# Kernel tuning notes

Hardware: AMD Instinct MI355X
Metric: run time of the kernel (lower is better)

Reference implementation:

```python
import jax, jax.numpy as jnp
import numpy as np

V, E, H, B, S = 50000, 256, 256, 64, 2048


def setup_inputs() -> dict:
    key = jax.random.key(0)
    ks = jax.random.split(key, 13)
    u = lambda k, shape: jax.random.uniform(k, shape, jnp.float32) - 0.5
    return {
        "inp": jax.random.randint(ks[0], (B,), 0, V, dtype=jnp.int64),
        "hidden": jax.random.normal(ks[1], (1, B, H), jnp.float32),
        "encoder_outputs": jax.random.normal(ks[2], (B, S, H), jnp.float32),
        "emb": jax.random.normal(ks[3], (V, E), jnp.float32),          # nn.Embedding weight
        "U": u(ks[4], (H, H)),
        "W": u(ks[5], (H, H)),
        "v": u(ks[6], (H, 1)),
        "W_ih": u(ks[7], (H, E)),   # RNN weight_ih_l0
        "W_hh": u(ks[8], (H, H)),   # RNN weight_hh_l0
        "b_ih": u(ks[9], (H,)),
        "b_hh": u(ks[10], (H,)),
        "W_out": u(ks[11], (V, H)),  # output Linear weight
        "b_out": u(ks[12], (V,)),
    }


def reference(inp, hidden, encoder_outputs, emb, U, W, v,
              W_ih, W_hh, b_ih, b_hh, W_out, b_out):
    # embedding lookup: (B, E)
    x = emb[inp]
    word_embs = x[:, None, :]                         # (B, 1, E)
    # Bahdanau additive attention (get_context)
    summed = jnp.tanh(word_embs @ U + encoder_outputs @ W)   # (B, S, H)
    e_ij = summed @ v                                        # (B, S, 1)
    alpha = jax.nn.softmax(e_ij, axis=1)                     # (B, S, 1)
    context = jnp.sum(alpha * encoder_outputs, axis=1)       # (B, H)
    # single tanh-RNN step; NOTE: original code feeds context as initial hidden,
    # ignoring the `hidden` argument when attention is enabled.
    h_new = jnp.tanh(x @ W_ih.T + b_ih + context @ W_hh.T + b_hh)  # (B, H)
    logits = h_new @ W_out.T + b_out                               # (B, V)
    return logits, h_new[None]                                     # hidden: (1, B, H)
```

## Files before the change

### kernel.cpp

```cpp
#include <hip/hip_runtime.h>
#include <hip/hip_bf16.h>
#include <math.h>

#define V_ 50000
#define E_ 256
#define H_ 256
#define B_ 64
#define S_ 2048
#define NCHK 32

typedef __attribute__((ext_vector_type(4))) float f32x4;
typedef __attribute__((ext_vector_type(16))) float f32x16;
typedef __attribute__((ext_vector_type(8))) __bf16 bf16x8;

static __device__ __forceinline__ f32x4 mfma16(bf16x8 a, bf16x8 b, f32x4 c) {
  return __builtin_amdgcn_mfma_f32_16x16x32_bf16(a, b, c, 0, 0, 0);
}
static __device__ __forceinline__ f32x16 mfma32(bf16x8 a, bf16x8 b, f32x16 c) {
  return __builtin_amdgcn_mfma_f32_32x32x16_bf16(a, b, c, 0, 0, 0);
}
static __device__ __forceinline__ float fast_tanh(float x) {
  const float e2 = __expf(2.0f * x);
  return 1.0f - 2.0f / (e2 + 1.0f);
}

__global__ __launch_bounds__(256) void prep_k(
    const int* __restrict__ inp, const float* __restrict__ emb,
    const float* __restrict__ U, const float* __restrict__ W_ih,
    const float* __restrict__ b_ih, const float* __restrict__ b_hh,
    float* __restrict__ xU, float* __restrict__ xWih) {
  const int b = blockIdx.x, h = threadIdx.x;
  __shared__ float xs[H_];
  xs[h] = emb[(size_t)inp[b] * E_ + h];
  __syncthreads();
  float au = 0.f, aw = 0.f;
  const float* __restrict__ wir = W_ih + (size_t)h * E_;
  for (int k = 0; k < H_; k += 4) {
    const float4 x4 = *reinterpret_cast<const float4*>(&xs[k]);
    const float4 w4 = *reinterpret_cast<const float4*>(wir + k);
    aw = fmaf(x4.x, w4.x, aw); aw = fmaf(x4.y, w4.y, aw);
    aw = fmaf(x4.z, w4.z, aw); aw = fmaf(x4.w, w4.w, aw);
    au = fmaf(x4.x, U[(size_t)(k + 0) * H_ + h], au);
    au = fmaf(x4.y, U[(size_t)(k + 1) * H_ + h], au);
    au = fmaf(x4.z, U[(size_t)(k + 2) * H_ + h], au);
    au = fmaf(x4.w, U[(size_t)(k + 3) * H_ + h], au);
  }
  xU[b * H_ + h] = au;
  xWih[b * H_ + h] = aw + b_ih[h] + b_hh[h];
}

__global__ __launch_bounds__(256) void prep_w(
    const float* __restrict__ W, __bf16* __restrict__ wt2) {
  const int idx = blockIdx.x * 256 + threadIdx.x;
  const int k = idx >> 8, col = idx & 255;
  wt2[((size_t)(k >> 3) * 256 + col) * 8 + (k & 7)] = (__bf16)W[(size_t)k * H_ + col];
}

__global__ __launch_bounds__(512, 4) void attn_fused(
    const float* __restrict__ enc, const __bf16* __restrict__ wt2,
    const float* __restrict__ xU, const float* __restrict__ vv,
    float* __restrict__ ctxp, float* __restrict__ mlout) {
  const int t = threadIdx.x;
  const int w = t >> 6, l = t & 63, l31 = l & 31, h5 = l >> 5;
  const int rg = w >> 1, cg = w & 1;

  __shared__ float ered[2][128];
  __shared__ float wgt[2][64];
  __shared__ float mlL[2][2];

  const int ridx = blockIdx.x;
  const int b = blockIdx.y;
  const int s0 = ridx * 128;

  const float* __restrict__ encA =
      enc + ((size_t)b * S_ + s0 + rg * 32 + l31) * H_ + h5 * 8;

  f32x16 acc[4];
#pragma unroll
  for (int cf = 0; cf < 4; ++cf) acc[cf] = (f32x16)(0.f);

  float4 af[2][2];
  af[0][0] = *reinterpret_cast<const float4*>(encA);
  af[0][1] = *reinterpret_cast<const float4*>(encA + 4);
  af[1][0] = *reinterpret_cast<const float4*>(encA + 16);
  af[1][1] = *reinterpret_cast<const float4*>(encA + 20);

#pragma unroll
  for (int ks = 0; ks < 16; ++ks) {
    const int ca = ks & 1;
    bf16x8 ahi, alo;
    {
      const float4 c0 = af[ca][0], c1 = af[ca][1];
      const float xa[8] = {c0.x, c0.y, c0.z, c0.w, c1.x, c1.y, c1.z, c1.w};
#pragma unroll
      for (int j = 0; j < 8; ++j) {
        const __bf16 hh = (__bf16)xa[j];
        ahi[j] = hh;
        alo[j] = (__bf16)(xa[j] - (float)hh);
      }
    }
    if (ks < 14) {
      af[ca][0] = *reinterpret_cast<const float4*>(encA + (ks + 2) * 16);
      af[ca][1] = *reinterpret_cast<const float4*>(encA + (ks + 2) * 16 + 4);
    }
    bf16x8 bb[4];
    const int koct = ks * 2 + h5;
#pragma unroll
    for (int cf = 0; cf < 4; ++cf)
      bb[cf] = *reinterpret_cast<const bf16x8*>(
          wt2 + ((size_t)koct * 256 + cg * 128 + cf * 32 + l31) * 8);
#pragma unroll
    for (int cf = 0; cf < 4; ++cf) acc[cf] = mfma32(ahi, bb[cf], acc[cf]);
#pragma unroll
    for (int cf = 0; cf < 4; ++cf) acc[cf] = mfma32(alo, bb[cf], acc[cf]);
  }

  float xu[4], vw[4];
#pragma unroll
  for (int cf = 0; cf < 4; ++cf) {
    const int col = cg * 128 + cf * 32 + l31;
    xu[cf] = xU[b * H_ + col];
    vw[cf] = vv[col];
  }
  float rs[16];
#pragma unroll
  for (int reg = 0; reg < 16; ++reg) {
    float s = 0.f;
#pragma unroll
    for (int cf = 0; cf < 4; ++cf)
      s += fast_tanh(xu[cf] + acc[cf][reg]) * vw[cf];
    rs[reg] = s;
  }
#pragma unroll
  for (int o = 1; o < 32; o <<= 1)
#pragma unroll
    for (int reg = 0; reg < 16; ++reg)
      rs[reg] += __shfl_xor(rs[reg], o);
  if (l31 == 0) {
#pragma unroll
    for (int reg = 0; reg < 16; ++reg)
      ered[cg][rg * 32 + (reg & 3) + 8 * (reg >> 2) + 4 * h5] = rs[reg];
  }
  __syncthreads();

  if (t < 128) {
    const int cc = t >> 6, rr = t & 63;
    const float es = ered[0][cc * 64 + rr] + ered[1][cc * 64 + rr];
    float m = es;
#pragma unroll
    for (int o = 1; o < 64; o <<= 1) m = fmaxf(m, __shfl_xor(m, o));
    const float we = __expf(es - m);
    float ls = we;
#pragma unroll
    for (int o = 1; o < 64; o <<= 1) ls += __shfl_xor(ls, o);
    wgt[cc][rr] = we;
    if (rr == 0) { mlL[cc][0] = m; mlL[cc][1] = ls; }
  }
  __syncthreads();

  {
    const int cc = t >> 8, h = t & 255;
    const float* __restrict__ ep = enc + ((size_t)b * S_ + s0 + cc * 64) * H_ + h;
    float a = 0.f;
#pragma unroll 8
    for (int s = 0; s < 64; ++s) a = fmaf(wgt[cc][s], ep[(size_t)s * H_], a);
    ctxp[((size_t)(ridx * 2 + cc) * B_ + b) * H_ + h] = a;
  }
  if (t < 4) {
    const int cc = t >> 1;
    mlout[((ridx * 2 + cc) * B_ + b) * 2 + (t & 1)] = mlL[cc][t & 1];
  }
}

__global__ __launch_bounds__(256) void combine_hnew(
    const float* __restrict__ ctxp, const float* __restrict__ mlout,
    const float* __restrict__ xWih, const float* __restrict__ W_hh,
    float* __restrict__ out_h, __bf16* __restrict__ hn) {
  const int b = blockIdx.x, h = threadIdx.x;
  __shared__ float cs[H_];
  float M = -3.4e38f;
#pragma unroll
  for (int cc = 0; cc < NCHK; ++cc) M = fmaxf(M, mlout[(cc * B_ + b) * 2]);
  float num = 0.f, den = 0.f;
#pragma unroll
  for (int cc = 0; cc < NCHK; ++cc) {
    const float mw = __expf(mlout[(cc * B_ + b) * 2] - M);
    den = fmaf(mw, mlout[(cc * B_ + b) * 2 + 1], den);
    num = fmaf(mw, ctxp[((size_t)cc * B_ + b) * H_ + h], num);
  }
  cs[h] = num / den;
  __syncthreads();
  const float* __restrict__ wr = W_hh + (size_t)h * H_;
  float a = xWih[b * H_ + h];
  for (int k = 0; k < H_; k += 4) {
    const float4 w4 = *reinterpret_cast<const float4*>(wr + k);
    const float4 c4 = *reinterpret_cast<const float4*>(&cs[k]);
    a = fmaf(c4.x, w4.x, a); a = fmaf(c4.y, w4.y, a);
    a = fmaf(c4.z, w4.z, a); a = fmaf(c4.w, w4.w, a);
  }
  const float hv = fast_tanh(a);
  out_h[b * H_ + h] = hv;
  hn[b * H_ + h] = (__bf16)hv;
}

__global__ __launch_bounds__(256) void logits_mfma(
    const float* __restrict__ Wout, const float* __restrict__ bout,
    const __bf16* __restrict__ hn, float* __restrict__ logits) {
  const int v0 = blockIdx.x * 64;
  const int t = threadIdx.x;
  const int wv = t >> 6, l = t & 63, l15 = l & 15, lg = l >> 4;

  __shared__ __bf16 Wsub[8][64][32];

  {
    const int srow = t >> 2, sg = t & 3;
    const int wslot = (sg + (srow >> 1)) & 3;
    const int vc = (v0 + srow) < V_ ? (v0 + srow) : (V_ - 1);
    const float* __restrict__ wr = Wout + (size_t)vc * H_ + sg * 8;
#pragma unroll
    for (int ks = 0; ks < 8; ++ks) {
      const float4 f0 = *reinterpret_cast<const float4*>(wr + ks * 32);
      const float4 f1 = *reinterpret_cast<const float4*>(wr + ks * 32 + 4);
      const float xv[8] = {f0.x, f0.y, f0.z, f0.w, f1.x, f1.y, f1.z, f1.w};
      bf16x8 h8;
#pragma unroll
      for (int j = 0; j < 8; ++j) h8[j] = (__bf16)xv[j];
      *reinterpret_cast<bf16x8*>(&Wsub[ks][srow][wslot * 8]) = h8;
    }
  }
  __syncthreads();

  f32x4 acc[4];
#pragma unroll
  for (int i = 0; i < 4; ++i) acc[i] = (f32x4)(0.f);
  const int colb = wv * 16 + l15;
#pragma unroll
  for (int k = 0; k < 8; ++k) {
    const bf16x8 bfrag = *reinterpret_cast<const bf16x8*>(hn + (size_t)colb * H_ + k * 32 + lg * 8);
    bf16x8 ah[4];
#pragma unroll
    for (int rf = 0; rf < 4; ++rf) {
      const int rr = rf * 16 + l15;
      const int slot = (lg + (rr >> 1)) & 3;
      ah[rf] = *reinterpret_cast<const bf16x8*>(&Wsub[k][rr][slot * 8]);
    }
#pragma unroll
    for (int rf = 0; rf < 4; ++rf)
      acc[rf] = mfma16(ah[rf], bfrag, acc[rf]);
  }
#pragma unroll
  for (int rf = 0; rf < 4; ++rf) {
    const int v = v0 + rf * 16 + lg * 4;
    if (v < V_) {
      const float4 bo = *reinterpret_cast<const float4*>(bout + v);
      float4 o;
      o.x = acc[rf][0] + bo.x; o.y = acc[rf][1] + bo.y;
      o.z = acc[rf][2] + bo.z; o.w = acc[rf][3] + bo.w;
      *reinterpret_cast<float4*>(logits + (size_t)colb * V_ + v) = o;
    }
  }
}

extern "C" void kernel_launch(void* const* d_in, const int* in_sizes, int n_in,
                              void* d_out, int out_size, void* d_ws, size_t ws_size,
                              hipStream_t stream) {
  const int*   inp  = (const int*)  d_in[0];
  const float* enc  = (const float*)d_in[2];
  const float* emb  = (const float*)d_in[3];
  const float* U    = (const float*)d_in[4];
  const float* W    = (const float*)d_in[5];
  const float* v    = (const float*)d_in[6];
  const float* W_ih = (const float*)d_in[7];
  const float* W_hh = (const float*)d_in[8];
  const float* b_ih = (const float*)d_in[9];
  const float* b_hh = (const float*)d_in[10];
  const float* Wout = (const float*)d_in[11];
  const float* bout = (const float*)d_in[12];

  float* logits = (float*)d_out;
  float* out_h  = logits + (size_t)B_ * V_;

  float* ws    = (float*)d_ws;
  __bf16* wt2  = (__bf16*)ws;
  float* xU    = ws + 32768;
  float* xWih  = xU + B_ * H_;
  float* ctxp  = xWih + B_ * H_;
  float* mlout = ctxp + (size_t)NCHK * B_ * H_;
  __bf16* hn   = (__bf16*)(mlout + NCHK * B_ * 2);

  prep_k<<<dim3(B_), dim3(256), 0, stream>>>(inp, emb, U, W_ih, b_ih, b_hh, xU, xWih);
  prep_w<<<dim3(H_ * H_ / 256), dim3(256), 0, stream>>>(W, wt2);
  attn_fused<<<dim3(16, B_), dim3(512), 0, stream>>>(enc, wt2, xU, v, ctxp, mlout);
  combine_hnew<<<dim3(B_), dim3(256), 0, stream>>>(ctxp, mlout, xWih, W_hh, out_h, hn);
  logits_mfma<<<dim3((V_ + 63) / 64), dim3(256), 0, stream>>>(Wout, bout, hn, logits);
}
```

Measured before the change: 116.2 us.

## Stage encoder tiles through LDS ring with async global_load_lds and smaller blocks

The attention kernel now streams encoder-output K-slices into a 4-deep LDS ring buffer with XOR swizzling, using direct global-to-LDS loads and explicit vmcnt waits plus barriers. It also double-buffers the bf16 W fragments in registers. Blocks shrink from 512 threads covering 128 rows to 256 threads covering 64 rows, with twice as many blocks along the sequence. The goal is to hide global-load latency behind the MFMA work and raise occupancy. In exchange it adds a barrier per K-step and fragile hand-tuned waitcnt counts.

Measured after the change: 105.4 us. -9.3%, faster.

```diff
diff --git a/kernel.cpp b/kernel.cpp
--- a/kernel.cpp
+++ b/kernel.cpp
@@ -22,6 +22,11 @@
 static __device__ __forceinline__ float fast_tanh(float x) {
   const float e2 = __expf(2.0f * x);
   return 1.0f - 2.0f / (e2 + 1.0f);
+}
+static __device__ __forceinline__ void gll16(const float* g, void* l) {
+  __builtin_amdgcn_global_load_lds(
+      (const __attribute__((address_space(1))) void*)g,
+      (__attribute__((address_space(3))) void*)l, 16, 0, 0);
 }
 
 __global__ __launch_bounds__(256) void prep_k(
@@ -56,7 +61,8 @@
   wt2[((size_t)(k >> 3) * 256 + col) * 8 + (k & 7)] = (__bf16)W[(size_t)k * H_ + col];
 }
 
-__global__ __launch_bounds__(512, 4) void attn_fused(
+#define SLAB 4096
+__global__ __launch_bounds__(256, 3) void attn_fused(
     const float* __restrict__ enc, const __bf16* __restrict__ wt2,
     const float* __restrict__ xU, const float* __restrict__ vv,
     float* __restrict__ ctxp, float* __restrict__ mlout) {
@@ -64,34 +70,64 @@
   const int w = t >> 6, l = t & 63, l31 = l & 31, h5 = l >> 5;
   const int rg = w >> 1, cg = w & 1;
 
-  __shared__ float ered[2][128];
-  __shared__ float wgt[2][64];
-  __shared__ float mlL[2][2];
+  __shared__ __align__(16) char Aring[4 * SLAB];
+  __shared__ float ered[2][64];
+  __shared__ float wgt[64];
+  __shared__ float mlS[2];
 
   const int ridx = blockIdx.x;
   const int b = blockIdx.y;
-  const int s0 = ridx * 128;
-
-  const float* __restrict__ encA =
-      enc + ((size_t)b * S_ + s0 + rg * 32 + l31) * H_ + h5 * 8;
+  const int s0 = ridx * 64;
+
+  const int srow = w * 16 + (l >> 2);
+  const int pch = l & 3;
+  const int kch = pch ^ ((srow >> 1) & 3);
+  const float* __restrict__ encSrc = enc + ((size_t)b * S_ + s0 + srow) * H_ + kch * 4;
+
+#define STAGE(ks_)                                                   \
+  gll16(encSrc + (ks_) * 16, Aring + ((ks_) & 3) * SLAB + w * 1024); \
+  __builtin_amdgcn_sched_barrier(0);
+
+  STAGE(0); STAGE(1); STAGE(2);
+  bf16x8 bh[2][4], bl2[2][4];
+#pragma unroll
+  for (int cf = 0; cf < 4; ++cf) {
+    const int col = cg * 128 + cf * 32 + l31;
+    bh[0][cf] = *reinterpret_cast<const bf16x8*>(wt2 + ((size_t)h5 * 256 + col) * 8);
+  }
 
   f32x16 acc[4];
 #pragma unroll
   for (int cf = 0; cf < 4; ++cf) acc[cf] = (f32x16)(0.f);
 
-  float4 af[2][2];
-  af[0][0] = *reinterpret_cast<const float4*>(encA);
-  af[0][1] = *reinterpret_cast<const float4*>(encA + 4);
-  af[1][0] = *reinterpret_cast<const float4*>(encA + 16);
-  af[1][1] = *reinterpret_cast<const float4*>(encA + 20);
+  const int r = rg * 32 + l31;
+  const int sxor = (r >> 1) & 3;
+  const char* arow = Aring + r * 64;
 
 #pragma unroll
   for (int ks = 0; ks < 16; ++ks) {
-    const int ca = ks & 1;
+    if (ks <= 13)      asm volatile("s_waitcnt vmcnt(6)" ::: "memory");
+    else if (ks == 14) asm volatile("s_waitcnt vmcnt(5)" ::: "memory");
+    else               asm volatile("s_waitcnt vmcnt(4)" ::: "memory");
+    __builtin_amdgcn_s_barrier();
+    __builtin_amdgcn_sched_barrier(0);
+    if (ks <= 12) { STAGE(ks + 3); }
+    const int pb = ks & 1;
+    if (ks < 15) {
+      const int koct = (ks + 1) * 2 + h5;
+#pragma unroll
+      for (int cf = 0; cf < 4; ++cf) {
+        const int col = cg * 128 + cf * 32 + l31;
+        bh[pb ^ 1][cf] = *reinterpret_cast<const bf16x8*>(
+            wt2 + ((size_t)koct * 256 + col) * 8);
+      }
+    }
+    const char* sb = arow + (ks & 3) * SLAB;
+    const f32x4 c0 = *reinterpret_cast<const f32x4*>(sb + (((2 * h5 + 0) ^ sxor) << 4));
+    const f32x4 c1 = *reinterpret_cast<const f32x4*>(sb + (((2 * h5 + 1) ^ sxor) << 4));
     bf16x8 ahi, alo;
     {
-      const float4 c0 = af[ca][0], c1 = af[ca][1];
-      const float xa[8] = {c0.x, c0.y, c0.z, c0.w, c1.x, c1.y, c1.z, c1.w};
+      const float xa[8] = {c0[0], c0[1], c0[2], c0[3], c1[0], c1[1], c1[2], c1[3]};
 #pragma unroll
       for (int j = 0; j < 8; ++j) {
         const __bf16 hh = (__bf16)xa[j];
@@ -99,21 +135,12 @@
         alo[j] = (__bf16)(xa[j] - (float)hh);
       }
     }
-    if (ks < 14) {
-      af[ca][0] = *reinterpret_cast<const float4*>(encA + (ks + 2) * 16);
-      af[ca][1] = *reinterpret_cast<const float4*>(encA + (ks + 2) * 16 + 4);
-    }
-    bf16x8 bb[4];
-    const int koct = ks * 2 + h5;
-#pragma unroll
-    for (int cf = 0; cf < 4; ++cf)
-      bb[cf] = *reinterpret_cast<const bf16x8*>(
-          wt2 + ((size_t)koct * 256 + cg * 128 + cf * 32 + l31) * 8);
-#pragma unroll
-    for (int cf = 0; cf < 4; ++cf) acc[cf] = mfma32(ahi, bb[cf], acc[cf]);
-#pragma unroll
-    for (int cf = 0; cf < 4; ++cf) acc[cf] = mfma32(alo, bb[cf], acc[cf]);
-  }
+#pragma unroll
+    for (int cf = 0; cf < 4; ++cf) acc[cf] = mfma32(ahi, bh[pb][cf], acc[cf]);
+#pragma unroll
+    for (int cf = 0; cf < 4; ++cf) acc[cf] = mfma32(alo, bh[pb][cf], acc[cf]);
+  }
+#undef STAGE
 
   float xu[4], vw[4];
 #pragma unroll
@@ -143,9 +170,8 @@
   }
   __syncthreads();
 
-  if (t < 128) {
-    const int cc = t >> 6, rr = t & 63;
-    const float es = ered[0][cc * 64 + rr] + ered[1][cc * 64 + rr];
+  if (t < 64) {
+    const float es = ered[0][t] + ered[1][t];
     float m = es;
 #pragma unroll
     for (int o = 1; o < 64; o <<= 1) m = fmaxf(m, __shfl_xor(m, o));
@@ -153,23 +179,19 @@
     float ls = we;
 #pragma unroll
     for (int o = 1; o < 64; o <<= 1) ls += __shfl_xor(ls, o);
-    wgt[cc][rr] = we;
-    if (rr == 0) { mlL[cc][0] = m; mlL[cc][1] = ls; }
+    wgt[t] = we;
+    if (t == 0) { mlS[0] = m; mlS[1] = ls; }
   }
   __syncthreads();
 
   {
-    const int cc = t >> 8, h = t & 255;
-    const float* __restrict__ ep = enc + ((size_t)b * S_ + s0 + cc * 64) * H_ + h;
+    const float* __restrict__ ep = enc + ((size_t)b * S_ + s0) * H_ + t;
     float a = 0.f;
 #pragma unroll 8
-    for (int s = 0; s < 64; ++s) a = fmaf(wgt[cc][s], ep[(size_t)s * H_], a);
-    ctxp[((size_t)(ridx * 2 + cc) * B_ + b) * H_ + h] = a;
-  }
-  if (t < 4) {
-    const int cc = t >> 1;
-    mlout[((ridx * 2 + cc) * B_ + b) * 2 + (t & 1)] = mlL[cc][t & 1];
-  }
+    for (int s = 0; s < 64; ++s) a = fmaf(wgt[s], ep[(size_t)s * H_], a);
+    ctxp[((size_t)ridx * B_ + b) * H_ + t] = a;
+  }
+  if (t < 2) mlout[(ridx * B_ + b) * 2 + t] = mlS[t];
 }
 
 __global__ __launch_bounds__(256) void combine_hnew(
@@ -290,7 +312,7 @@
 
   prep_k<<<dim3(B_), dim3(256), 0, stream>>>(inp, emb, U, W_ih, b_ih, b_hh, xU, xWih);
   prep_w<<<dim3(H_ * H_ / 256), dim3(256), 0, stream>>>(W, wt2);
-  attn_fused<<<dim3(16, B_), dim3(512), 0, stream>>>(enc, wt2, xU, v, ctxp, mlout);
+  attn_fused<<<dim3(NCHK, B_), dim3(256), 0, stream>>>(enc, wt2, xU, v, ctxp, mlout);
   combine_hnew<<<dim3(B_), dim3(256), 0, stream>>>(ctxp, mlout, xWih, W_hh, out_h, hn);
   logits_mfma<<<dim3((V_ + 63) / 64), dim3(256), 0, stream>>>(Wout, bout, hn, logits);
 }
```
